# Optimization experiments

Measured on AMD Instinct MI355X. Metric: run time of the kernel, lower is better.

## Reference

```python
import jax, jax.numpy as jnp
import numpy as np

SIGMA = 1.0  # RBF kernel bandwidth


def _rbf(a, b, sigma=SIGMA):
    # a: [N, d], b: [M, d] -> Gram matrix [N, M]
    # squared pairwise distances via ||a||^2 + ||b||^2 - 2 a.b
    a2 = jnp.sum(a * a, axis=-1)[:, None]          # [N, 1]
    b2 = jnp.sum(b * b, axis=-1)[None, :]          # [1, M]
    d2 = a2 + b2 - 2.0 * (a @ b.T)                 # [N, M]
    d2 = jnp.maximum(d2, 0.0)
    return jnp.exp(-d2 / (2.0 * sigma * sigma))


def setup_inputs() -> dict:
    key = jax.random.key(0)
    kx, kw = jax.random.split(key)
    x = jax.random.normal(kx, (8192, 3), dtype=jnp.float32)
    w = jax.random.normal(kw, (8192, 3), dtype=jnp.float32)  # learned point cloud param
    return {"x": x, "w": w}


def reference(x, w):
    # ImpCloudMMD.__call__: mean k(w,w) - 2 mean k(x,w) + mean k(x,x)
    t1 = jnp.mean(_rbf(w, w))
    t2 = 2.0 * jnp.mean(_rbf(x, w))
    t3 = jnp.mean(_rbf(x, x))
    return t1 - t2 + t3
```

## Files before the change

kernel.cpp:

```cpp
#include <hip/hip_runtime.h>
#include <hip/hip_bf16.h>


#define NPTS   8192
#define CH     256
#define NC     64
#define NXC    32
#define NB     2080
#define BLOCK  256
#define CEXP   (-0.72134752044448169f)
#define M2CEXP (1.44269504088896340736f)

typedef float f32x2 __attribute__((ext_vector_type(2)));
typedef float f32x4 __attribute__((ext_vector_type(4)));

__device__ __forceinline__ f32x2 pkfma(f32x2 a, f32x2 b, f32x2 c) {
#if __has_builtin(__builtin_elementwise_fma)
    return __builtin_elementwise_fma(a, b, c);
#else
    f32x2 r; r.x = fmaf(a.x, b.x, c.x); r.y = fmaf(a.y, b.y, c.y); return r;
#endif
}

__device__ __forceinline__ float fexp2(float v) {
#if __has_builtin(__builtin_amdgcn_exp2f)
    return __builtin_amdgcn_exp2f(v);
#else
    float r;
    asm("v_exp_f32 %0, %1" : "=v"(r) : "v"(v));
    return r;
#endif
}

__global__ __launch_bounds__(BLOCK, 6) void mmd_tri(const float* __restrict__ x,
                                                    const float* __restrict__ w,
                                                    float* __restrict__ partials) {
    __shared__ f32x4  sAX[CH/4], sAY[CH/4], sAZ[CH/4], sA2[CH/4];
    __shared__ float4 sB[CH];
    __shared__ float  red[4];

    const int bid = blockIdx.x;
    int I = (int)((sqrtf(8.0f * (float)bid + 1.0f) - 1.0f) * 0.5f);
    while ((I + 1) * (I + 2) / 2 <= bid) ++I;
    while (I * (I + 1) / 2 > bid) --I;
    const int J = bid - I * (I + 1) / 2;

    const int tid = threadIdx.x;
    {
        int gi = I * CH + tid;
        const float* s = (gi < NPTS) ? x : w;
        int ii = gi & (NPTS - 1);
        float px = s[3*ii], py = s[3*ii+1], pz = s[3*ii+2];
        ((float*)sAX)[tid] = M2CEXP * px;
        ((float*)sAY)[tid] = M2CEXP * py;
        ((float*)sAZ)[tid] = M2CEXP * pz;
        ((float*)sA2)[tid] = CEXP * (px*px + py*py + pz*pz);

        int gj = J * CH + tid;
        const float* t = (gj < NPTS) ? x : w;
        int jj = gj & (NPTS - 1);
        float qx = t[3*jj], qy = t[3*jj+1], qz = t[3*jj+2];
        sB[tid] = make_float4(qx, qy, qz, CEXP * (qx*qx + qy*qy + qz*qz));
    }
    __syncthreads();

    const int lane = tid & 63;
    const int wave = tid >> 6;

    f32x2 acc2[4];
#pragma unroll
    for (int p = 0; p < 4; ++p) acc2[p] = (f32x2){0.0f, 0.0f};

#pragma unroll 1
    for (int ai = 0; ai < CH / 32; ++ai) {
        const int a4 = (ai * 32 + wave * 8) >> 2;
        f32x4 ax0 = sAX[a4], ax1 = sAX[a4 + 1];
        f32x4 ay0 = sAY[a4], ay1 = sAY[a4 + 1];
        f32x4 az0 = sAZ[a4], az1 = sAZ[a4 + 1];
        f32x4 a20 = sA2[a4], a21 = sA2[a4 + 1];
        f32x2 axp[4] = { ax0.xy, ax0.zw, ax1.xy, ax1.zw };
        f32x2 ayp[4] = { ay0.xy, ay0.zw, ay1.xy, ay1.zw };
        f32x2 azp[4] = { az0.xy, az0.zw, az1.xy, az1.zw };
        f32x2 a2p[4] = { a20.xy, a20.zw, a21.xy, a21.zw };

#pragma unroll
        for (int k = 0; k < CH / 64; ++k) {
            float4 b = sB[k * 64 + lane];
            f32x2 bxx = { b.x, b.x };
            f32x2 byy = { b.y, b.y };
            f32x2 bzz = { b.z, b.z };
            f32x2 bww = { b.w, b.w };
#pragma unroll
            for (int p = 0; p < 4; ++p) {
                f32x2 arg = pkfma(axp[p], bxx,
                            pkfma(ayp[p], byy,
                            pkfma(azp[p], bzz, a2p[p] + bww)));
                f32x2 ev;
                ev.x = fexp2(arg.x);
                ev.y = fexp2(arg.y);
                acc2[p] += ev;
            }
        }
    }

    float tot = 0.0f;
#pragma unroll
    for (int p = 0; p < 4; ++p) tot += acc2[p].x + acc2[p].y;
#pragma unroll
    for (int off = 32; off > 0; off >>= 1)
        tot += __shfl_xor(tot, off, 64);

    if (lane == 0) red[wave] = tot;
    __syncthreads();
    if (tid == 0) {
        const float sa = (I < NXC) ? -1.0f : 1.0f;
        const float sb = (J < NXC) ? -1.0f : 1.0f;
        const float wt = (I == J) ? 1.0f : 2.0f;
        partials[bid] = (sa * sb * wt) * ((red[0] + red[1]) + (red[2] + red[3]));
    }
}

__global__ __launch_bounds__(256) void mmd_reduce(const float* __restrict__ partials,
                                                  float* __restrict__ out) {
    __shared__ float red[4];
    const int tid = threadIdx.x;
    float v = 0.0f;
    for (int i = tid; i < NB; i += 256) v += partials[i];
#pragma unroll
    for (int off = 32; off > 0; off >>= 1)
        v += __shfl_xor(v, off, 64);
    if ((tid & 63) == 0) red[tid >> 6] = v;
    __syncthreads();
    if (tid == 0)
        out[0] = ((red[0] + red[1]) + (red[2] + red[3])) * (1.0f / 67108864.0f);
}

extern "C" void kernel_launch(void* const* d_in, const int* in_sizes, int n_in,
                              void* d_out, int out_size, void* d_ws, size_t ws_size,
                              hipStream_t stream) {
    const float* x = (const float*)d_in[0];
    const float* w = (const float*)d_in[1];
    float* out      = (float*)d_out;
    float* partials = (float*)d_ws;

    hipLaunchKernelGGL(mmd_tri, dim3(NB), dim3(BLOCK), 0, stream, x, w, partials);
    hipLaunchKernelGGL(mmd_reduce, dim3(1), dim3(256), 0, stream, partials, out);
}
```

Before: 30.61 us.

## Factor B-norm exponential out of inner loop and split tiles into half-blocks

```diff
diff --git a/kernel.cpp b/kernel.cpp
--- a/kernel.cpp
+++ b/kernel.cpp
@@ -2,14 +2,15 @@
 #include <hip/hip_bf16.h>
 
 
-#define NPTS   8192
-#define CH     256
-#define NC     64
-#define NXC    32
-#define NB     2080
-#define BLOCK  256
-#define CEXP   (-0.72134752044448169f)
-#define M2CEXP (1.44269504088896340736f)
+#define NPTS     8192
+#define CH       256
+#define NC       64
+#define NXC      32
+#define NB_TILES 2080
+#define NB_UNITS 4160
+#define BLOCK    256
+#define CEXP     (-0.72134752044448169f)
+#define M2CEXP   (1.44269504088896340736f)
 
 typedef float f32x2 __attribute__((ext_vector_type(2)));
 typedef float f32x4 __attribute__((ext_vector_type(4)));
@@ -32,6 +33,8 @@
 #endif
 }
 
+#define PK2(v) ((f32x2){(v), (v)})
+
 __global__ __launch_bounds__(BLOCK, 6) void mmd_tri(const float* __restrict__ x,
                                                     const float* __restrict__ w,
                                                     float* __restrict__ partials) {
@@ -39,11 +42,14 @@
     __shared__ float4 sB[CH];
     __shared__ float  red[4];
 
-    const int bid = blockIdx.x;
-    int I = (int)((sqrtf(8.0f * (float)bid + 1.0f) - 1.0f) * 0.5f);
-    while ((I + 1) * (I + 2) / 2 <= bid) ++I;
-    while (I * (I + 1) / 2 > bid) --I;
-    const int J = bid - I * (I + 1) / 2;
+    const int unit = blockIdx.x;
+    const int tile = unit >> 1;
+    const int half = unit & 1;
+
+    int I = (int)((sqrtf(8.0f * (float)tile + 1.0f) - 1.0f) * 0.5f);
+    while ((I + 1) * (I + 2) / 2 <= tile) ++I;
+    while (I * (I + 1) / 2 > tile) --I;
+    const int J = tile - I * (I + 1) / 2;
 
     const int tid = threadIdx.x;
     {
@@ -60,7 +66,8 @@
         const float* t = (gj < NPTS) ? x : w;
         int jj = gj & (NPTS - 1);
         float qx = t[3*jj], qy = t[3*jj+1], qz = t[3*jj+2];
-        sB[tid] = make_float4(qx, qy, qz, CEXP * (qx*qx + qy*qy + qz*qz));
+        sB[tid] = make_float4(qx, qy, qz,
+                              fexp2(CEXP * (qx*qx + qy*qy + qz*qz)));
     }
     __syncthreads();
 
@@ -69,10 +76,10 @@
 
     f32x2 acc2[4];
 #pragma unroll
-    for (int p = 0; p < 4; ++p) acc2[p] = (f32x2){0.0f, 0.0f};
+    for (int p = 0; p < 4; ++p) acc2[p] = PK2(0.0f);
 
 #pragma unroll 1
-    for (int ai = 0; ai < CH / 32; ++ai) {
+    for (int ai = half * 4; ai < half * 4 + 4; ++ai) {
         const int a4 = (ai * 32 + wave * 8) >> 2;
         f32x4 ax0 = sAX[a4], ax1 = sAX[a4 + 1];
         f32x4 ay0 = sAY[a4], ay1 = sAY[a4 + 1];
@@ -86,19 +93,19 @@
 #pragma unroll
         for (int k = 0; k < CH / 64; ++k) {
             float4 b = sB[k * 64 + lane];
-            f32x2 bxx = { b.x, b.x };
-            f32x2 byy = { b.y, b.y };
-            f32x2 bzz = { b.z, b.z };
-            f32x2 bww = { b.w, b.w };
+            f32x2 bxx = PK2(b.x);
+            f32x2 byy = PK2(b.y);
+            f32x2 bzz = PK2(b.z);
+            f32x2 ebw = PK2(b.w);
 #pragma unroll
             for (int p = 0; p < 4; ++p) {
                 f32x2 arg = pkfma(axp[p], bxx,
                             pkfma(ayp[p], byy,
-                            pkfma(azp[p], bzz, a2p[p] + bww)));
+                            pkfma(azp[p], bzz, a2p[p])));
                 f32x2 ev;
                 ev.x = fexp2(arg.x);
                 ev.y = fexp2(arg.y);
-                acc2[p] += ev;
+                acc2[p] = pkfma(ev, ebw, acc2[p]);
             }
         }
     }
@@ -116,7 +123,7 @@
         const float sa = (I < NXC) ? -1.0f : 1.0f;
         const float sb = (J < NXC) ? -1.0f : 1.0f;
         const float wt = (I == J) ? 1.0f : 2.0f;
-        partials[bid] = (sa * sb * wt) * ((red[0] + red[1]) + (red[2] + red[3]));
+        partials[unit] = (sa * sb * wt) * ((red[0] + red[1]) + (red[2] + red[3]));
     }
 }
 
@@ -125,7 +132,7 @@
     __shared__ float red[4];
     const int tid = threadIdx.x;
     float v = 0.0f;
-    for (int i = tid; i < NB; i += 256) v += partials[i];
+    for (int i = tid; i < NB_UNITS; i += 256) v += partials[i];
 #pragma unroll
     for (int off = 32; off > 0; off >>= 1)
         v += __shfl_xor(v, off, 64);
@@ -143,6 +150,6 @@
     float* out      = (float*)d_out;
     float* partials = (float*)d_ws;
 
-    hipLaunchKernelGGL(mmd_tri, dim3(NB), dim3(BLOCK), 0, stream, x, w, partials);
+    hipLaunchKernelGGL(mmd_tri, dim3(NB_UNITS), dim3(BLOCK), 0, stream, x, w, partials);
     hipLaunchKernelGGL(mmd_reduce, dim3(1), dim3(256), 0, stream, partials, out);
 }
```

After: 30.47 us. No clear change (-0.4%).
